# Kernel optimization log

Hardware: AMD Instinct MI355X
Metric: run time of the kernel (lower is better)

## Reference

```python
import jax, jax.numpy as jnp
import numpy as np
from jax import lax


def setup_inputs() -> dict:
    key = jax.random.key(0)
    k1, k2, k3, k4 = jax.random.split(key, 4)
    bs, depth, h, w = 32, 512, 28, 28
    out_c, kh, kw = 512, 3, 3
    x = jax.random.uniform(k1, (bs, depth, h, w), dtype=jnp.float32)
    weight = jax.random.normal(k2, (out_c, depth, kh, kw), dtype=jnp.float32) * 0.02
    bias = jax.random.normal(k3, (out_c,), dtype=jnp.float32) * 0.02
    mask_weight = jax.random.uniform(k4, (depth,), dtype=jnp.float32)
    filt = jnp.ones((depth, 1), dtype=jnp.float32)  # filter==1 -> channel is masked
    return {"x": x, "weight": weight, "bias": bias, "mask_weight": mask_weight,
            "filter": filt, "padding": 1}


def _get_mu(x):
    # x: [bs, depth, h, w]; coordinates are 1-based as in the torch code
    bs, depth, h, w = x.shape
    ix = jnp.arange(1, h + 1, dtype=x.dtype).reshape(1, 1, h, 1)  # row coord
    iy = jnp.arange(1, w + 1, dtype=x.dtype).reshape(1, 1, 1, w)  # col coord
    sumX = jnp.maximum(x.sum((2, 3)), 1e-9)                       # [bs, depth]
    mu_x = jnp.maximum(jnp.round((ix * x).sum((2, 3)) / sumX), 1.0)
    mu_y = jnp.maximum(jnp.round((iy * x).sum((2, 3)) / sumX), 1.0)
    # map integer centroid (1..h) to linspace(-1, 1, h); original uses h for both axes
    lin = jnp.linspace(-1.0, 1.0, h, dtype=x.dtype)
    mu_xg = lin[(mu_x - 1.0).astype(jnp.int32)]                   # [bs, depth]
    mu_yg = lin[(mu_y - 1.0).astype(jnp.int32)]
    return mu_xg, mu_yg


def _get_mask(x, mask_weight, filt):
    bs, depth, h, w = x.shape
    mu_x, mu_y = _get_mu(x)                                        # [bs, depth] each
    posX = jnp.linspace(-1.0, 1.0, h, dtype=x.dtype).reshape(1, 1, h, 1)
    posY = jnp.linspace(-1.0, 1.0, w, dtype=x.dtype).reshape(1, 1, 1, w)
    m = jnp.abs(posX - mu_x[:, :, None, None]) + jnp.abs(posY - mu_y[:, :, None, None])
    m = 1.0 - m * mask_weight.reshape(1, depth, 1, 1)
    m = jnp.maximum(m, -1.0)
    # channels whose filter entry != 1 are unmasked (mask forced to 1)
    m = jnp.where(filt.reshape(1, depth, 1, 1) == 1.0, m, 1.0)
    return m


def reference(x, weight, bias, mask_weight, filter, padding):
    mask = _get_mask(x, mask_weight, filter)
    x_relu = jnp.maximum(x * mask, 0.0)
    out = lax.conv_general_dilated(
        x_relu, weight,
        window_strides=(1, 1),
        padding=[(padding, padding), (padding, padding)],
        dimension_numbers=("NCHW", "OIHW", "NCHW"))
    return out + bias.reshape(1, -1, 1, 1)
```

## Files before the change

### kernel.cpp

```cpp
#include <hip/hip_runtime.h>
#include <stdint.h>

typedef unsigned short u16;
typedef __attribute__((ext_vector_type(8))) short bf16x8;
typedef __attribute__((ext_vector_type(4))) float f32x4;

#define NB 32
#define CH 512
#define HP 30
#define KTOT 4608
#define BM 256
#define BN 224
#define BK 64
#define ABYTES 32768
#define BBYTES 28672
#define BUFU16 30720
#define KSTEPS 72

__device__ __forceinline__ u16 f2bf(float f) {
    uint32_t u = __float_as_uint(f);
    uint32_t r = (u + 0x7fffu + ((u >> 16) & 1u)) >> 16;
    return (u16)r;
}

__global__ __launch_bounds__(256) void stats_kernel(
    const float* __restrict__ x, float* __restrict__ muX, float* __restrict__ muY)
{
    int pair = blockIdx.x * 4 + (threadIdx.x >> 6);
    int lane = threadIdx.x & 63;
    const float* xp = x + (size_t)pair * 784;
    float s = 0.f, sx = 0.f, sy = 0.f;
    for (int e = lane; e < 784; e += 64) {
        float v = xp[e];
        int i = e / 28, j = e - i * 28;
        s += v;
        sx += (float)(i + 1) * v;
        sy += (float)(j + 1) * v;
    }
    #pragma unroll
    for (int off = 32; off > 0; off >>= 1) {
        s  += __shfl_down(s, off);
        sx += __shfl_down(sx, off);
        sy += __shfl_down(sy, off);
    }
    if (lane == 0) {
        float S = fmaxf(s, 1e-9f);
        float mx = fmaxf(rintf(sx / S), 1.0f);
        float my = fmaxf(rintf(sy / S), 1.0f);
        int ix = (int)(mx - 1.0f); if (ix > 27) ix = 27;
        int iy = (int)(my - 1.0f); if (iy > 27) iy = 27;
        muX[pair] = -1.0f + (2.0f / 27.0f) * (float)ix;
        muY[pair] = -1.0f + (2.0f / 27.0f) * (float)iy;
    }
}

#define TSTR 520
__global__ __launch_bounds__(256) void mask_relu_transpose(
    const float* __restrict__ x, const float* __restrict__ mw,
    const float* __restrict__ filt, const float* __restrict__ muX,
    const float* __restrict__ muY, u16* __restrict__ xr_pad)
{
    __shared__ u16 tile[28 * TSTR];
    int bid = blockIdx.x;
    int b = bid / 28, i = bid - (bid / 28) * 28;
    int tid = threadIdx.x;
    float px = -1.0f + (2.0f / 27.0f) * (float)i;
    const float* xb = x + (size_t)b * CH * 784 + i * 28;
    const float* muXb = muX + b * CH;
    const float* muYb = muY + b * CH;
    #pragma unroll 8
    for (int k = 0; k < 56; ++k) {
        int e = tid + k * 256;
        int c = e / 28, j = e - c * 28;
        float v = xb[c * 784 + j];
        float py = -1.0f + (2.0f / 27.0f) * (float)j;
        float m = 1.0f - (fabsf(px - muXb[c]) + fabsf(py - muYb[c])) * mw[c];
        m = fmaxf(m, -1.0f);
        if (filt[c] != 1.0f) m = 1.0f;
        tile[j * TSTR + c] = f2bf(fmaxf(v * m, 0.0f));
    }
    __syncthreads();
    u16* outb = xr_pad + (((size_t)b * HP + (i + 1)) * HP + 1) * CH;
    #pragma unroll
    for (int k = 0; k < 7; ++k) {
        int ch = tid + k * 256;
        int j = ch >> 6;
        int c0 = (ch & 63) << 3;
        *reinterpret_cast<uint4*>(outb + (size_t)j * CH + c0) =
            *reinterpret_cast<const uint4*>(&tile[j * TSTR + c0]);
    }
}

__global__ __launch_bounds__(256) void weight_reorder(
    const float* __restrict__ w, u16* __restrict__ w_r)
{
    __shared__ u16 t[KTOT];
    int oc = blockIdx.x;
    const float* wrow = w + (size_t)oc * KTOT;
    int tid = threadIdx.x;
    #pragma unroll
    for (int k = 0; k < 18; ++k) {
        int idx = tid + k * 256;
        int ic = idx / 9, tap = idx - ic * 9;
        t[tap * 512 + ic] = f2bf(wrow[idx]);
    }
    __syncthreads();
    u16* dst = w_r + (size_t)oc * KTOT;
    #pragma unroll
    for (int k = 0; k < 3; ++k) {
        int ch = tid + k * 256;
        if (ch < 576)
            *reinterpret_cast<uint4*>(dst + ch * 8) =
                *reinterpret_cast<const uint4*>(&t[ch * 8]);
    }
}

__global__ __launch_bounds__(512, 2) void conv_gemm(
    const u16* __restrict__ w_r, const u16* __restrict__ xr_pad,
    const float* __restrict__ bias, float* __restrict__ out)
{
    __shared__ __align__(16) u16 smem[2][BUFU16];
    int p = blockIdx.x;
    int bid = (p & 7) * 28 + (p >> 3);
    int mt = bid / 112, nt = bid - mt * 112;
    int m0 = mt * 256;
    int n0 = nt * 224;
    int tid = threadIdx.x;
    int lane = tid & 63;
    int w = tid >> 6;
    int wm = w >> 1, wn = w & 1;

    uint32_t aoff[4], boff[4], ldsA[4], ldsB[4];
    bool bmask[4];
    #pragma unroll
    for (int it = 0; it < 4; ++it) {
        int c = tid * 16 + it * 8192;
        int row = c >> 7;
        int scol = (c & 127) ^ ((row & 7) << 4);
        aoff[it] = (uint32_t)(m0 + row) * KTOT + (scol >> 1);
        ldsA[it] = c >> 1;
        bmask[it] = (c < BBYTES);
        int rb = (row < BN) ? row : 0;
        int n = n0 + rb;
        int b2 = n / 784, s2 = n - b2 * 784;
        int oh = s2 / 28, ow = s2 - oh * 28;
        boff[it] = (uint32_t)(((b2 * HP + oh) * HP + ow) * CH) + (scol >> 1);
        ldsB[it] = (ABYTES >> 1) + (uint32_t)((c < BBYTES ? c : 0) >> 1);
    }

    auto stage = [&](int buf, int ks) {
        u16* sA = smem[buf];
        u16* sB = smem[buf] + (ABYTES >> 1);
        int koff = ks * 64;
        int tap = ks >> 3;
        int kh = tap / 3, kw = tap - kh * 3;
        int xoff = (kh * HP + kw) * CH + (ks & 7) * 64;
        #pragma unroll
        for (int it = 0; it < 4; ++it) {
            __builtin_amdgcn_global_load_lds(
                (const __attribute__((address_space(1))) uint32_t*)(w_r + aoff[it] + koff),
                (__attribute__((address_space(3))) uint32_t*)(sA + ldsA[it]),
                16, 0, 0);
        }
        #pragma unroll
        for (int it = 0; it < 4; ++it) {
            if (bmask[it]) {
                __builtin_amdgcn_global_load_lds(
                    (const __attribute__((address_space(1))) uint32_t*)(xr_pad + boff[it] + xoff),
                    (__attribute__((address_space(3))) uint32_t*)(sB + (ldsB[it] - (ABYTES >> 1))),
                    16, 0, 0);
            }
        }
    };

    f32x4 acc[4][7];
    #pragma unroll
    for (int m = 0; m < 4; ++m)
        #pragma unroll
        for (int ni = 0; ni < 7; ++ni)
            acc[m][ni] = (f32x4){0.f, 0.f, 0.f, 0.f};

    int r15 = lane & 15;
    int rq = lane >> 4;
    int xorv = (r15 & 7) << 4;
    int cb0 = ((rq * 16) ^ xorv) >> 1;
    int cb1 = ((rq * 16 + 64) ^ xorv) >> 1;
    int arow = (wm * 64 + r15) * 64;
    int brow = (ABYTES >> 1) + (wn * 112 + r15) * 64;

    stage(0, 0);
    for (int ks = 0; ks < KSTEPS; ++ks) {
        __syncthreads();
        if (ks + 1 < KSTEPS) stage((ks + 1) & 1, ks + 1);
        const u16* sm = smem[ks & 1];
        #pragma unroll
        for (int kk = 0; kk < 2; ++kk) {
            int cb = kk ? cb1 : cb0;
            bf16x8 a[4];
            #pragma unroll
            for (int m = 0; m < 4; ++m)
                a[m] = *reinterpret_cast<const bf16x8*>(sm + arow + m * 1024 + cb);
            #pragma unroll
            for (int ni = 0; ni < 7; ++ni) {
                bf16x8 bv = *reinterpret_cast<const bf16x8*>(sm + brow + ni * 1024 + cb);
                #pragma unroll
                for (int m = 0; m < 4; ++m)
                    acc[m][ni] = __builtin_amdgcn_mfma_f32_16x16x32_bf16(a[m], bv, acc[m][ni], 0, 0, 0);
            }
        }
    }

    #pragma unroll
    for (int m = 0; m < 4; ++m) {
        int row = m0 + wm * 64 + m * 16 + rq * 4;
        #pragma unroll
        for (int ni = 0; ni < 7; ++ni) {
            int n = n0 + wn * 112 + ni * 16 + r15;
            int b2 = n / 784, s2 = n - b2 * 784;
            float* op = out + ((size_t)b2 * CH + row) * 784 + s2;
            f32x4 v = acc[m][ni];
            #pragma unroll
            for (int r = 0; r < 4; ++r)
                op[(size_t)r * 784] = v[r] + bias[row + r];
        }
    }
}

extern "C" void kernel_launch(void* const* d_in, const int* in_sizes, int n_in,
                              void* d_out, int out_size, void* d_ws, size_t ws_size,
                              hipStream_t stream)
{
    const float* x    = (const float*)d_in[0];
    const float* wgt  = (const float*)d_in[1];
    const float* bias = (const float*)d_in[2];
    const float* mw   = (const float*)d_in[3];
    const float* filt = (const float*)d_in[4];

    const size_t XR_BYTES = (size_t)NB * HP * HP * CH * 2;
    const size_t WR_BYTES = (size_t)CH * KTOT * 2;
    u16* xr_pad = (u16*)d_ws;
    u16* w_r    = (u16*)((char*)d_ws + XR_BYTES);
    float* muX  = (float*)((char*)d_ws + XR_BYTES + WR_BYTES);
    float* muY  = (float*)((char*)d_ws + XR_BYTES + WR_BYTES + 65536);

    hipMemsetAsync(xr_pad, 0, XR_BYTES, stream);
    hipLaunchKernelGGL(stats_kernel, dim3(4096), dim3(256), 0, stream, x, muX, muY);
    hipLaunchKernelGGL(mask_relu_transpose, dim3(NB * 28), dim3(256), 0, stream,
                       x, mw, filt, muX, muY, xr_pad);
    hipLaunchKernelGGL(weight_reorder, dim3(512), dim3(256), 0, stream, wgt, w_r);
    hipLaunchKernelGGL(conv_gemm, dim3(224), dim3(512), 0, stream,
                       w_r, xr_pad, bias, (float*)d_out);
}
```

Before: 248.7 us.

## Split GEMM K-step into ping-pong phases with barriers, priority boosts and split prefetch

Restructures the conv GEMM main loop into four phases per K-step. Each phase loads its LDS fragments, synchronises the block, and then runs its MFMAs at raised wave priority. The A and B global-to-LDS prefetches are issued in separate phases, which spreads memory traffic across the compute, and an explicit vmcnt wait plus barrier closes each step. The aim is to interleave loads and MFMAs more regularly across waves, at the cost of many more barriers per iteration.

```diff
diff --git a/kernel.cpp b/kernel.cpp
--- a/kernel.cpp
+++ b/kernel.cpp
@@ -145,16 +145,12 @@
         int b2 = n / 784, s2 = n - b2 * 784;
         int oh = s2 / 28, ow = s2 - oh * 28;
         boff[it] = (uint32_t)(((b2 * HP + oh) * HP + ow) * CH) + (scol >> 1);
-        ldsB[it] = (ABYTES >> 1) + (uint32_t)((c < BBYTES ? c : 0) >> 1);
-    }
-
-    auto stage = [&](int buf, int ks) {
+        ldsB[it] = (uint32_t)((c < BBYTES ? c : 0) >> 1);
+    }
+
+    auto stageA = [&](int buf, int ks) {
         u16* sA = smem[buf];
-        u16* sB = smem[buf] + (ABYTES >> 1);
         int koff = ks * 64;
-        int tap = ks >> 3;
-        int kh = tap / 3, kw = tap - kh * 3;
-        int xoff = (kh * HP + kw) * CH + (ks & 7) * 64;
         #pragma unroll
         for (int it = 0; it < 4; ++it) {
             __builtin_amdgcn_global_load_lds(
@@ -162,12 +158,18 @@
                 (__attribute__((address_space(3))) uint32_t*)(sA + ldsA[it]),
                 16, 0, 0);
         }
+    };
+    auto stageB = [&](int buf, int ks) {
+        u16* sB = smem[buf] + (ABYTES >> 1);
+        int tap = ks >> 3;
+        int kh = tap / 3, kw = tap - kh * 3;
+        int xoff = (kh * HP + kw) * CH + (ks & 7) * 64;
         #pragma unroll
         for (int it = 0; it < 4; ++it) {
             if (bmask[it]) {
                 __builtin_amdgcn_global_load_lds(
                     (const __attribute__((address_space(1))) uint32_t*)(xr_pad + boff[it] + xoff),
-                    (__attribute__((address_space(3))) uint32_t*)(sB + (ldsB[it] - (ABYTES >> 1))),
+                    (__attribute__((address_space(3))) uint32_t*)(sB + ldsB[it]),
                     16, 0, 0);
             }
         }
@@ -188,26 +190,88 @@
     int arow = (wm * 64 + r15) * 64;
     int brow = (ABYTES >> 1) + (wn * 112 + r15) * 64;
 
-    stage(0, 0);
+    stageA(0, 0);
+    stageB(0, 0);
+    __syncthreads();
+
     for (int ks = 0; ks < KSTEPS; ++ks) {
-        __syncthreads();
-        if (ks + 1 < KSTEPS) stage((ks + 1) & 1, ks + 1);
         const u16* sm = smem[ks & 1];
-        #pragma unroll
-        for (int kk = 0; kk < 2; ++kk) {
-            int cb = kk ? cb1 : cb0;
-            bf16x8 a[4];
+        const int nbuf = (ks + 1) & 1;
+        const bool pf = (ks + 1 < KSTEPS);
+
+        if (pf) stageA(nbuf, ks + 1);
+        bf16x8 a0[4], bA[4];
+        #pragma unroll
+        for (int m = 0; m < 4; ++m)
+            a0[m] = *reinterpret_cast<const bf16x8*>(sm + arow + m * 1024 + cb0);
+        #pragma unroll
+        for (int ni = 0; ni < 4; ++ni)
+            bA[ni] = *reinterpret_cast<const bf16x8*>(sm + brow + ni * 1024 + cb0);
+        __builtin_amdgcn_s_barrier();
+        asm volatile("s_waitcnt lgkmcnt(0)" ::: "memory");
+        __builtin_amdgcn_sched_barrier(0);
+        __builtin_amdgcn_s_setprio(1);
+        #pragma unroll
+        for (int ni = 0; ni < 4; ++ni)
             #pragma unroll
             for (int m = 0; m < 4; ++m)
-                a[m] = *reinterpret_cast<const bf16x8*>(sm + arow + m * 1024 + cb);
-            #pragma unroll
-            for (int ni = 0; ni < 7; ++ni) {
-                bf16x8 bv = *reinterpret_cast<const bf16x8*>(sm + brow + ni * 1024 + cb);
-                #pragma unroll
-                for (int m = 0; m < 4; ++m)
-                    acc[m][ni] = __builtin_amdgcn_mfma_f32_16x16x32_bf16(a[m], bv, acc[m][ni], 0, 0, 0);
-            }
-        }
+                acc[m][ni] = __builtin_amdgcn_mfma_f32_16x16x32_bf16(a0[m], bA[ni], acc[m][ni], 0, 0, 0);
+        __builtin_amdgcn_s_setprio(0);
+        __builtin_amdgcn_s_barrier();
+
+        if (pf) stageB(nbuf, ks + 1);
+        bf16x8 bB[3];
+        #pragma unroll
+        for (int ni = 0; ni < 3; ++ni)
+            bB[ni] = *reinterpret_cast<const bf16x8*>(sm + brow + (ni + 4) * 1024 + cb0);
+        __builtin_amdgcn_s_barrier();
+        asm volatile("s_waitcnt lgkmcnt(0)" ::: "memory");
+        __builtin_amdgcn_sched_barrier(0);
+        __builtin_amdgcn_s_setprio(1);
+        #pragma unroll
+        for (int ni = 0; ni < 3; ++ni)
+            #pragma unroll
+            for (int m = 0; m < 4; ++m)
+                acc[m][ni + 4] = __builtin_amdgcn_mfma_f32_16x16x32_bf16(a0[m], bB[ni], acc[m][ni + 4], 0, 0, 0);
+        __builtin_amdgcn_s_setprio(0);
+        __builtin_amdgcn_s_barrier();
+
+        bf16x8 a1[4], bC[4];
+        #pragma unroll
+        for (int m = 0; m < 4; ++m)
+            a1[m] = *reinterpret_cast<const bf16x8*>(sm + arow + m * 1024 + cb1);
+        #pragma unroll
+        for (int ni = 0; ni < 4; ++ni)
+            bC[ni] = *reinterpret_cast<const bf16x8*>(sm + brow + ni * 1024 + cb1);
+        __builtin_amdgcn_s_barrier();
+        asm volatile("s_waitcnt lgkmcnt(0)" ::: "memory");
+        __builtin_amdgcn_sched_barrier(0);
+        __builtin_amdgcn_s_setprio(1);
+        #pragma unroll
+        for (int ni = 0; ni < 4; ++ni)
+            #pragma unroll
+            for (int m = 0; m < 4; ++m)
+                acc[m][ni] = __builtin_amdgcn_mfma_f32_16x16x32_bf16(a1[m], bC[ni], acc[m][ni], 0, 0, 0);
+        __builtin_amdgcn_s_setprio(0);
+        __builtin_amdgcn_s_barrier();
+
+        bf16x8 bD[3];
+        #pragma unroll
+        for (int ni = 0; ni < 3; ++ni)
+            bD[ni] = *reinterpret_cast<const bf16x8*>(sm + brow + (ni + 4) * 1024 + cb1);
+        __builtin_amdgcn_s_barrier();
+        asm volatile("s_waitcnt lgkmcnt(0)" ::: "memory");
+        __builtin_amdgcn_sched_barrier(0);
+        __builtin_amdgcn_s_setprio(1);
+        #pragma unroll
+        for (int ni = 0; ni < 3; ++ni)
+            #pragma unroll
+            for (int m = 0; m < 4; ++m)
+                acc[m][ni + 4] = __builtin_amdgcn_mfma_f32_16x16x32_bf16(a1[m], bD[ni], acc[m][ni + 4], 0, 0, 0);
+        __builtin_amdgcn_s_setprio(0);
+        asm volatile("s_waitcnt vmcnt(0)" ::: "memory");
+        __builtin_amdgcn_sched_barrier(0);
+        __builtin_amdgcn_s_barrier();
     }
 
     #pragma unroll
```

New measurement: 255.3 us. 1.03x slower.

## Load weight operand directly from global into registers, stage only activations in LDS

Applied to the files above, without the earlier changes.

The conv GEMM no longer copies the weight tile into shared memory. Each wave reads its A fragments for the current k-step directly from global memory into registers, while the activation tile stays double-buffered in LDS. The goal is to halve LDS footprint and LDS traffic, which could raise occupancy and reduce ds_read pressure. In exchange, the A loads have unhidden global latency within each iteration, and each weight element is read by both N-side waves, which adds redundant global/L2 traffic.

```diff
diff --git a/kernel.cpp b/kernel.cpp
--- a/kernel.cpp
+++ b/kernel.cpp
@@ -12,9 +12,7 @@
 #define BM 256
 #define BN 224
 #define BK 64
-#define ABYTES 32768
-#define BBYTES 28672
-#define BUFU16 30720
+#define BNU16 14336
 #define KSTEPS 72
 
 __device__ __forceinline__ u16 f2bf(float f) {
@@ -119,7 +117,7 @@
     const u16* __restrict__ w_r, const u16* __restrict__ xr_pad,
     const float* __restrict__ bias, float* __restrict__ out)
 {
-    __shared__ __align__(16) u16 smem[2][BUFU16];
+    __shared__ __align__(16) u16 smem[2][BNU16];
     int p = blockIdx.x;
     int bid = (p & 7) * 28 + (p >> 3);
     int mt = bid / 112, nt = bid - mt * 112;
@@ -129,45 +127,36 @@
     int lane = tid & 63;
     int w = tid >> 6;
     int wm = w >> 1, wn = w & 1;
-
-    uint32_t aoff[4], boff[4], ldsA[4], ldsB[4];
+    int r15 = lane & 15;
+    int rq = lane >> 4;
+
+    uint32_t boff[4], ldsB[4];
     bool bmask[4];
     #pragma unroll
     for (int it = 0; it < 4; ++it) {
-        int c = tid * 16 + it * 8192;
+        int ch = tid + it * 512;
+        bmask[it] = (ch < 1792);
+        int c = (bmask[it] ? ch : 0) * 16;
         int row = c >> 7;
         int scol = (c & 127) ^ ((row & 7) << 4);
-        aoff[it] = (uint32_t)(m0 + row) * KTOT + (scol >> 1);
-        ldsA[it] = c >> 1;
-        bmask[it] = (c < BBYTES);
-        int rb = (row < BN) ? row : 0;
-        int n = n0 + rb;
+        int n = n0 + row;
         int b2 = n / 784, s2 = n - b2 * 784;
         int oh = s2 / 28, ow = s2 - oh * 28;
         boff[it] = (uint32_t)(((b2 * HP + oh) * HP + ow) * CH) + (scol >> 1);
-        ldsB[it] = (ABYTES >> 1) + (uint32_t)((c < BBYTES ? c : 0) >> 1);
-    }
-
-    auto stage = [&](int buf, int ks) {
-        u16* sA = smem[buf];
-        u16* sB = smem[buf] + (ABYTES >> 1);
-        int koff = ks * 64;
+        ldsB[it] = c >> 1;
+    }
+
+    auto stageB = [&](int buf, int ks) {
+        u16* sB = smem[buf];
         int tap = ks >> 3;
         int kh = tap / 3, kw = tap - kh * 3;
         int xoff = (kh * HP + kw) * CH + (ks & 7) * 64;
-        #pragma unroll
-        for (int it = 0; it < 4; ++it) {
-            __builtin_amdgcn_global_load_lds(
-                (const __attribute__((address_space(1))) uint32_t*)(w_r + aoff[it] + koff),
-                (__attribute__((address_space(3))) uint32_t*)(sA + ldsA[it]),
-                16, 0, 0);
-        }
         #pragma unroll
         for (int it = 0; it < 4; ++it) {
             if (bmask[it]) {
                 __builtin_amdgcn_global_load_lds(
                     (const __attribute__((address_space(1))) uint32_t*)(xr_pad + boff[it] + xoff),
-                    (__attribute__((address_space(3))) uint32_t*)(sB + (ldsB[it] - (ABYTES >> 1))),
+                    (__attribute__((address_space(3))) uint32_t*)(sB + ldsB[it]),
                     16, 0, 0);
             }
         }
@@ -180,32 +169,37 @@
         for (int ni = 0; ni < 7; ++ni)
             acc[m][ni] = (f32x4){0.f, 0.f, 0.f, 0.f};
 
-    int r15 = lane & 15;
-    int rq = lane >> 4;
     int xorv = (r15 & 7) << 4;
     int cb0 = ((rq * 16) ^ xorv) >> 1;
     int cb1 = ((rq * 16 + 64) ^ xorv) >> 1;
-    int arow = (wm * 64 + r15) * 64;
-    int brow = (ABYTES >> 1) + (wn * 112 + r15) * 64;
-
-    stage(0, 0);
+    int brow = (wn * 112 + r15) * 64;
+
+    const u16* ap = w_r + (size_t)(m0 + wm * 64 + r15) * KTOT + rq * 8;
+
+    stageB(0, 0);
     for (int ks = 0; ks < KSTEPS; ++ks) {
         __syncthreads();
-        if (ks + 1 < KSTEPS) stage((ks + 1) & 1, ks + 1);
-        const u16* sm = smem[ks & 1];
+        const u16* apk = ap + ks * 64;
+        bf16x8 a0[4], a1[4];
+        #pragma unroll
+        for (int m = 0; m < 4; ++m)
+            a0[m] = *reinterpret_cast<const bf16x8*>(apk + (size_t)m * 16 * KTOT);
+        #pragma unroll
+        for (int m = 0; m < 4; ++m)
+            a1[m] = *reinterpret_cast<const bf16x8*>(apk + (size_t)m * 16 * KTOT + 32);
+        if (ks + 1 < KSTEPS) stageB((ks + 1) & 1, ks + 1);
+
+        const u16* sB = smem[ks & 1];
         #pragma unroll
         for (int kk = 0; kk < 2; ++kk) {
             int cb = kk ? cb1 : cb0;
-            bf16x8 a[4];
-            #pragma unroll
-            for (int m = 0; m < 4; ++m)
-                a[m] = *reinterpret_cast<const bf16x8*>(sm + arow + m * 1024 + cb);
             #pragma unroll
             for (int ni = 0; ni < 7; ++ni) {
-                bf16x8 bv = *reinterpret_cast<const bf16x8*>(sm + brow + ni * 1024 + cb);
+                bf16x8 bv = *reinterpret_cast<const bf16x8*>(sB + brow + ni * 1024 + cb);
                 #pragma unroll
                 for (int m = 0; m < 4; ++m)
-                    acc[m][ni] = __builtin_amdgcn_mfma_f32_16x16x32_bf16(a[m], bv, acc[m][ni], 0, 0, 0);
+                    acc[m][ni] = __builtin_amdgcn_mfma_f32_16x16x32_bf16(
+                        kk ? a1[m] : a0[m], bv, acc[m][ni], 0, 0, 0);
             }
         }
     }
```

Measured after the change: 350.3 us. +40.8%, slower.
